# Kernel optimization log

Measured on AMD Instinct MI355X. Metric: run time of the kernel, lower is better.

The kernel has to match this reference:

```python
import jax, jax.numpy as jnp
import numpy as np

DXDY = (1.0, 0.0)        # init kwarg dxdy
DIM_KERNSIZE = 10        # init kwarg dim_kernsize -> 21 taps
PRECISION_FACTOR = 1.0   # forward default


def setup_inputs() -> dict:
    key = jax.random.key(0)
    k1, k2 = jax.random.split(key)
    B, C, H, W = 1, 3, 1024, 1024
    x = jax.random.normal(k1, (B, C, H, W), dtype=jnp.float32)
    # per-pixel sigma in [0.1, 5.1) so halfStepWidth varies across pixels
    sigma = jax.random.uniform(k2, (B, 1, H, W), dtype=jnp.float32) * 5.0 + 0.1
    return {"x": x, "sigma": sigma}


def _bilinear_sample(x, ys, xs):
    # x: [B,C,H,W]; ys, xs: [K2,H,W] float sample positions in pixel space.
    # Clamp-to-edge bilinear interpolation -> [B,C,K2,H,W]
    B, C, H, W = x.shape
    x0 = jnp.floor(xs)
    y0 = jnp.floor(ys)
    wx = xs - x0
    wy = ys - y0
    x0i = jnp.clip(x0.astype(jnp.int32), 0, W - 1)
    x1i = jnp.clip(x0i + 1, 0, W - 1)
    y0i = jnp.clip(y0.astype(jnp.int32), 0, H - 1)
    y1i = jnp.clip(y0i + 1, 0, H - 1)
    g = lambda yi, xi: x[:, :, yi, xi]  # gather -> [B,C,K2,H,W]
    return (g(y0i, x0i) * ((1.0 - wy) * (1.0 - wx))
            + g(y0i, x1i) * ((1.0 - wy) * wx)
            + g(y1i, x0i) * (wy * (1.0 - wx))
            + g(y1i, x1i) * (wy * wx))


def reference(x, sigma):
    B, C, H, W = x.shape
    K = DIM_KERNSIZE
    sig = sigma[:, None] * PRECISION_FACTOR          # i.view(sigma, dims=5): [B,1,1,H,W]
    two_sigma_sq = 2.0 * sig * sig
    half_step = jnp.ceil(2.0 * sig)                  # [B,1,1,H,W]
    itr = jnp.arange(-K, K + 1, dtype=jnp.float32).reshape(1, -1, 1, 1, 1)
    gk = jnp.exp(-itr * itr / two_sigma_sq)          # [B,K2,1,H,W]
    gk = jnp.where((itr >= -half_step) & (itr <= half_step), gk, 0.0)
    # sample positions: current pixel (add_p_start=True) + itr * dxdy (pixel units;
    # offsets = itr * dxdy / tex_size are normalized, multiplied back by tex_size here)
    it = jnp.arange(-K, K + 1, dtype=jnp.float32)
    gy, gx = jnp.meshgrid(jnp.arange(H, dtype=jnp.float32),
                          jnp.arange(W, dtype=jnp.float32), indexing="ij")
    xs = gx[None] + it[:, None, None] * DXDY[0]      # [K2,H,W]
    ys = gy[None] + it[:, None, None] * DXDY[1]
    s = _bilinear_sample(x, ys, xs)                  # [B,C,K2,H,W]
    s = jnp.transpose(s, (0, 2, 1, 3, 4))            # [B,K2,C,H,W]
    num = jnp.sum(s * gk, axis=1)                    # [B,C,H,W]
    norm = jnp.sum(gk, axis=1)                       # [B,1,H,W]
    # safe_div: 0 where norm == 0
    ok = norm > 0
    return jnp.where(ok, num / jnp.where(ok, norm, 1.0), 0.0)
```

## Files before the change

kernel.cpp:

```cpp
#include <hip/hip_runtime.h>
#include <math.h>


#define HH 1024
#define WW 1024
#define CC 3
#define KK 10
#define PP 4

__global__ __launch_bounds__(256) void gauss1d_kernel(
    const float* __restrict__ x,
    const float* __restrict__ sigma,
    float* __restrict__ out)
{
    const int t = blockIdx.x * blockDim.x + threadIdx.x;
    const int p0 = t * PP;
    const int h = p0 >> 10;
    const int w0 = p0 & (WW - 1);

    const float4 sg4 = *reinterpret_cast<const float4*>(sigma + p0);
    const float sgs[PP] = {sg4.x, sg4.y, sg4.z, sg4.w};
    float wts[PP][KK + 1];
    float inv_norm[PP];
    #pragma unroll
    for (int p = 0; p < PP; ++p) {
        const float sig = sgs[p];
        const float inv2s2 = __builtin_amdgcn_rcpf(2.0f * sig * sig);
        const float hs = ceilf(2.0f * sig);
        const float q = __expf(-inv2s2);
        const float q2 = q * q;
        float wp = 1.0f;
        float tq = q;
        float norm = 1.0f;
        wts[p][0] = 1.0f;
        #pragma unroll
        for (int i = 1; i <= KK; ++i) {
            float wi = wp * tq;
            tq *= q2;
            wi = ((float)i <= hs) ? wi : 0.0f;
            wts[p][i] = wi;
            norm += 2.0f * wi;
            wp = wi;
        }
        inv_norm[p] = __builtin_amdgcn_rcpf(norm);
    }

    const int base = w0 - 12;
    #pragma unroll
    for (int c = 0; c < CC; ++c) {
        const float* __restrict__ rc = x + c * (HH * WW) + h * WW;
        const float left  = rc[0];
        const float right = rc[WW - 1];
        float v[28];
        #pragma unroll
        for (int k = 0; k < 7; ++k) {
            const int bk = base + 4 * k;
            int bkc = bk < 0 ? 0 : bk;
            bkc = bkc > (WW - 4) ? (WW - 4) : bkc;
            float4 lv = *reinterpret_cast<const float4*>(rc + bkc);
            if (k < 3) {
                const bool cl = bk < 0;
                lv.x = cl ? left : lv.x;  lv.y = cl ? left : lv.y;
                lv.z = cl ? left : lv.z;  lv.w = cl ? left : lv.w;
            }
            if (k > 3) {
                const bool cr = bk > (WW - 4);
                lv.x = cr ? right : lv.x; lv.y = cr ? right : lv.y;
                lv.z = cr ? right : lv.z; lv.w = cr ? right : lv.w;
            }
            v[4 * k + 0] = lv.x; v[4 * k + 1] = lv.y;
            v[4 * k + 2] = lv.z; v[4 * k + 3] = lv.w;
        }

        float4 res;
        float* rp = reinterpret_cast<float*>(&res);
        #pragma unroll
        for (int p = 0; p < PP; ++p) {
            const int o = 12 + p;
            float acc = v[o];
            #pragma unroll
            for (int i = 1; i <= KK; ++i)
                acc += wts[p][i] * (v[o - i] + v[o + i]);
            rp[p] = acc * inv_norm[p];
        }
        *reinterpret_cast<float4*>(out + c * (HH * WW) + p0) = res;
    }
}

extern "C" void kernel_launch(void* const* d_in, const int* in_sizes, int n_in,
                              void* d_out, int out_size, void* d_ws, size_t ws_size,
                              hipStream_t stream) {
    const float* x = (const float*)d_in[0];
    const float* sigma = (const float*)d_in[1];
    float* out = (float*)d_out;

    const int n_threads = (HH * WW) / PP;
    const int block = 256;
    const int grid = n_threads / block;
    gauss1d_kernel<<<grid, block, 0, stream>>>(x, sigma, out);
}
```

Before: 12.09 us.

## Stage row tiles in shared memory with replicated edge padding

```diff
diff --git a/kernel.cpp b/kernel.cpp
--- a/kernel.cpp
+++ b/kernel.cpp
@@ -7,18 +7,51 @@
 #define CC 3
 #define KK 10
 #define PP 4
+#define PAD 12
+#define ROWLEN (WW + 2 * PAD)
 
 __global__ __launch_bounds__(256) void gauss1d_kernel(
     const float* __restrict__ x,
     const float* __restrict__ sigma,
     float* __restrict__ out)
 {
-    const int t = blockIdx.x * blockDim.x + threadIdx.x;
-    const int p0 = t * PP;
-    const int h = p0 >> 10;
-    const int w0 = p0 & (WW - 1);
+    __shared__ float smem[CC][ROWLEN];
 
+    const int tid = threadIdx.x;
+    const int h   = blockIdx.x;
+    const int w0  = tid * PP;
+    const int p0  = h * WW + w0;
+
+    float4 lv[CC];
+    #pragma unroll
+    for (int c = 0; c < CC; ++c)
+        lv[c] = *reinterpret_cast<const float4*>(x + c * (HH * WW) + h * WW + w0);
     const float4 sg4 = *reinterpret_cast<const float4*>(sigma + p0);
+
+    #pragma unroll
+    for (int c = 0; c < CC; ++c)
+        *reinterpret_cast<float4*>(&smem[c][PAD + w0]) = lv[c];
+    if (tid == 0) {
+        #pragma unroll
+        for (int c = 0; c < CC; ++c) {
+            const float e = lv[c].x;
+            const float4 pv = {e, e, e, e};
+            *reinterpret_cast<float4*>(&smem[c][0]) = pv;
+            *reinterpret_cast<float4*>(&smem[c][4]) = pv;
+            *reinterpret_cast<float4*>(&smem[c][8]) = pv;
+        }
+    }
+    if (tid == 255) {
+        #pragma unroll
+        for (int c = 0; c < CC; ++c) {
+            const float e = lv[c].w;
+            const float4 pv = {e, e, e, e};
+            *reinterpret_cast<float4*>(&smem[c][PAD + WW + 0]) = pv;
+            *reinterpret_cast<float4*>(&smem[c][PAD + WW + 4]) = pv;
+            *reinterpret_cast<float4*>(&smem[c][PAD + WW + 8]) = pv;
+        }
+    }
+
     const float sgs[PP] = {sg4.x, sg4.y, sg4.z, sg4.w};
     float wts[PP][KK + 1];
     float inv_norm[PP];
@@ -45,38 +78,22 @@
         inv_norm[p] = __builtin_amdgcn_rcpf(norm);
     }
 
-    const int base = w0 - 12;
+    __syncthreads();
+
     #pragma unroll
     for (int c = 0; c < CC; ++c) {
-        const float* __restrict__ rc = x + c * (HH * WW) + h * WW;
-        const float left  = rc[0];
-        const float right = rc[WW - 1];
         float v[28];
         #pragma unroll
         for (int k = 0; k < 7; ++k) {
-            const int bk = base + 4 * k;
-            int bkc = bk < 0 ? 0 : bk;
-            bkc = bkc > (WW - 4) ? (WW - 4) : bkc;
-            float4 lv = *reinterpret_cast<const float4*>(rc + bkc);
-            if (k < 3) {
-                const bool cl = bk < 0;
-                lv.x = cl ? left : lv.x;  lv.y = cl ? left : lv.y;
-                lv.z = cl ? left : lv.z;  lv.w = cl ? left : lv.w;
-            }
-            if (k > 3) {
-                const bool cr = bk > (WW - 4);
-                lv.x = cr ? right : lv.x; lv.y = cr ? right : lv.y;
-                lv.z = cr ? right : lv.z; lv.w = cr ? right : lv.w;
-            }
-            v[4 * k + 0] = lv.x; v[4 * k + 1] = lv.y;
-            v[4 * k + 2] = lv.z; v[4 * k + 3] = lv.w;
+            const float4 rv = *reinterpret_cast<const float4*>(&smem[c][w0 + 4 * k]);
+            v[4 * k + 0] = rv.x; v[4 * k + 1] = rv.y;
+            v[4 * k + 2] = rv.z; v[4 * k + 3] = rv.w;
         }
-
         float4 res;
         float* rp = reinterpret_cast<float*>(&res);
         #pragma unroll
         for (int p = 0; p < PP; ++p) {
-            const int o = 12 + p;
+            const int o = PAD + p;
             float acc = v[o];
             #pragma unroll
             for (int i = 1; i <= KK; ++i)
@@ -94,8 +111,7 @@
     const float* sigma = (const float*)d_in[1];
     float* out = (float*)d_out;
 
-    const int n_threads = (HH * WW) / PP;
+    const int grid = HH;
     const int block = 256;
-    const int grid = n_threads / block;
     gauss1d_kernel<<<grid, block, 0, stream>>>(x, sigma, out);
 }
```

After: 12.76 us. +5.5%, slower.

## Halve pixels per thread, add interior fast path, raise occupancy hint

Applied to the files above, without the earlier changes.

```diff
diff --git a/kernel.cpp b/kernel.cpp
--- a/kernel.cpp
+++ b/kernel.cpp
@@ -6,22 +6,22 @@
 #define WW 1024
 #define CC 3
 #define KK 10
-#define PP 4
+#define PP 2
 
-__global__ __launch_bounds__(256) void gauss1d_kernel(
+__global__ __launch_bounds__(256, 6) void gauss1d_kernel(
     const float* __restrict__ x,
     const float* __restrict__ sigma,
     float* __restrict__ out)
 {
-    const int t = blockIdx.x * blockDim.x + threadIdx.x;
-    const int p0 = t * PP;
-    const int h = p0 >> 10;
-    const int w0 = p0 & (WW - 1);
+    const int t  = blockIdx.x * blockDim.x + threadIdx.x;
+    const int h  = t >> 9;
+    const int w0 = (t & 511) * PP;
+    const int p0 = h * WW + w0;
 
-    const float4 sg4 = *reinterpret_cast<const float4*>(sigma + p0);
-    const float sgs[PP] = {sg4.x, sg4.y, sg4.z, sg4.w};
-    float wts[PP][KK + 1];
-    float inv_norm[PP];
+    const float2 sg = *reinterpret_cast<const float2*>(sigma + p0);
+    const float sgs[PP] = {sg.x, sg.y};
+    float wt[PP][KK];
+    float invn[PP];
     #pragma unroll
     for (int p = 0; p < PP; ++p) {
         const float sig = sgs[p];
@@ -32,58 +32,52 @@
         float wp = 1.0f;
         float tq = q;
         float norm = 1.0f;
-        wts[p][0] = 1.0f;
         #pragma unroll
         for (int i = 1; i <= KK; ++i) {
             float wi = wp * tq;
             tq *= q2;
             wi = ((float)i <= hs) ? wi : 0.0f;
-            wts[p][i] = wi;
+            wt[p][i - 1] = wi;
             norm += 2.0f * wi;
             wp = wi;
         }
-        inv_norm[p] = __builtin_amdgcn_rcpf(norm);
+        invn[p] = __builtin_amdgcn_rcpf(norm);
     }
 
+    const bool fast = (w0 >= 12) && (w0 <= WW - 12);
     const int base = w0 - 12;
+
     #pragma unroll
     for (int c = 0; c < CC; ++c) {
         const float* __restrict__ rc = x + c * (HH * WW) + h * WW;
-        const float left  = rc[0];
-        const float right = rc[WW - 1];
-        float v[28];
-        #pragma unroll
-        for (int k = 0; k < 7; ++k) {
-            const int bk = base + 4 * k;
-            int bkc = bk < 0 ? 0 : bk;
-            bkc = bkc > (WW - 4) ? (WW - 4) : bkc;
-            float4 lv = *reinterpret_cast<const float4*>(rc + bkc);
-            if (k < 3) {
-                const bool cl = bk < 0;
-                lv.x = cl ? left : lv.x;  lv.y = cl ? left : lv.y;
-                lv.z = cl ? left : lv.z;  lv.w = cl ? left : lv.w;
+        float v[24];
+        if (fast) {
+            const float* __restrict__ bp = rc + base;
+            #pragma unroll
+            for (int k = 0; k < 12; ++k) {
+                const float2 lv = *reinterpret_cast<const float2*>(bp + 2 * k);
+                v[2 * k]     = lv.x;
+                v[2 * k + 1] = lv.y;
             }
-            if (k > 3) {
-                const bool cr = bk > (WW - 4);
-                lv.x = cr ? right : lv.x; lv.y = cr ? right : lv.y;
-                lv.z = cr ? right : lv.z; lv.w = cr ? right : lv.w;
+        } else {
+            #pragma unroll
+            for (int j = 0; j < 24; ++j) {
+                int col = base + j;
+                col = col < 0 ? 0 : col;
+                col = col > (WW - 1) ? (WW - 1) : col;
+                v[j] = rc[col];
             }
-            v[4 * k + 0] = lv.x; v[4 * k + 1] = lv.y;
-            v[4 * k + 2] = lv.z; v[4 * k + 3] = lv.w;
         }
 
-        float4 res;
-        float* rp = reinterpret_cast<float*>(&res);
+        float a0 = v[12];
+        float a1 = v[13];
         #pragma unroll
-        for (int p = 0; p < PP; ++p) {
-            const int o = 12 + p;
-            float acc = v[o];
-            #pragma unroll
-            for (int i = 1; i <= KK; ++i)
-                acc += wts[p][i] * (v[o - i] + v[o + i]);
-            rp[p] = acc * inv_norm[p];
+        for (int i = 1; i <= KK; ++i) {
+            a0 += wt[0][i - 1] * (v[12 - i] + v[12 + i]);
+            a1 += wt[1][i - 1] * (v[13 - i] + v[13 + i]);
         }
-        *reinterpret_cast<float4*>(out + c * (HH * WW) + p0) = res;
+        const float2 res = {a0 * invn[0], a1 * invn[1]};
+        *reinterpret_cast<float2*>(out + c * (HH * WW) + p0) = res;
     }
 }
 
```

Result: slower. 24.25 us (+100.5%).
